# Performance work log

Measured on AMD Instinct MI355X. Metric: run time of the kernel, lower is better.

The kernel has to match this reference:

```python
import jax, jax.numpy as jnp
import numpy as np

IN_DIM = 256
HID = 384
HEADS = 6
NH1 = HID // HEADS  # 64 per-head hidden in layer1
N = 3072
SLOPE_GAT = 0.2   # LeakyReLU inside GAT attention
SLOPE_ACT = 0.01  # default nn.LeakyReLU / F.leaky_relu slope


def _leaky(x, s):
    return jnp.where(x >= 0, x, s * x)


def _gat_sublayer(h, mask, W, a, heads, nh, concat):
    # h: [N, F_in], mask: [N, N] bool, W: [heads*nh, F_in], a: [2*nh]
    n = h.shape[0]
    g = (h @ W.T).reshape(n, heads, nh)  # [N, H, F]
    # e[i,j,h] = leakyrelu(<g_i, a_l> + <g_j, a_r>)  (avoids O(N^2) concat)
    sl = jnp.einsum('nhf,f->nh', g, a[:nh])
    sr = jnp.einsum('nhf,f->nh', g, a[nh:])
    e = _leaky(sl[:, None, :] + sr[None, :, :], SLOPE_GAT)  # [N, N, H]
    e = jnp.where(mask[:, :, None], e, jnp.float32(-10000.0))
    att = jax.nn.softmax(e, axis=1)  # softmax over source nodes j
    out = jnp.einsum('ijh,jhf->ihf', att, g)
    return out.reshape(n, heads * nh) if concat else out.mean(axis=1)


def _gat(x, mask, W1, a1, W2, a2):
    x = _gat_sublayer(x, mask, W1, a1, HEADS, NH1, True)   # [N, HID]
    x = jax.nn.elu(x)
    return _gat_sublayer(x, mask, W2, a2, 1, IN_DIM, False)  # [N, IN_DIM]


def setup_inputs() -> dict:
    key = jax.random.key(0)
    ks = iter(jax.random.split(key, 32))
    d = {
        'feature': jax.random.normal(next(ks), (1, N, IN_DIM), jnp.float32),
        'adj': jax.random.randint(next(ks), (1, N, N), 0, 2, jnp.int32),
        'doc_num': 16,
        'sect_num': 192,
    }
    def w(shape, scale=0.05):
        return jax.random.normal(next(ks), shape, jnp.float32) * scale
    for br in ('sent', 'sect', 'doc'):
        d[f'W1_{br}'] = w((HID, IN_DIM))
        d[f'a1_{br}'] = w((2 * NH1,))
        d[f'W2_{br}'] = w((IN_DIM, HID))
        d[f'a2_{br}'] = w((2 * IN_DIM,))
    d['fusion_W'] = w((IN_DIM, 3 * IN_DIM)); d['fusion_b'] = jnp.zeros((IN_DIM,), jnp.float32)
    d['ffn_W0'] = w((HID, IN_DIM)); d['ffn_b0'] = jnp.zeros((HID,), jnp.float32)
    d['ffn_W1'] = w((HID, HID)); d['ffn_b1'] = jnp.zeros((HID,), jnp.float32)
    d['ffn_W2'] = w((IN_DIM, HID)); d['ffn_b2'] = jnp.zeros((IN_DIM,), jnp.float32)
    return d


def reference(feature, adj, doc_num, sect_num,
              W1_sent, a1_sent, W2_sent, a2_sent,
              W1_sect, a1_sect, W2_sect, a2_sect,
              W1_doc, a1_doc, W2_doc, a2_doc,
              fusion_W, fusion_b,
              ffn_W0, ffn_b0, ffn_W1, ffn_b1, ffn_W2, ffn_b2):
    f = feature[0]          # [N, D]
    n = f.shape[0]
    A = adj[0] != 0         # [N, N]
    cols = jnp.arange(n)
    sent_mask = A & (cols < n - sect_num - doc_num)[None, :]
    sect_mask = A & (cols >= n - sect_num - doc_num)[None, :] & (cols < n - doc_num)[None, :]
    doc_mask = A & (cols >= n - doc_num)[None, :]

    f_sent = _gat(f, sent_mask, W1_sent, a1_sent, W2_sent, a2_sent) + f
    f_sect = _gat(f, sect_mask, W1_sect, a1_sect, W2_sect, a2_sect) + f
    f_doc = _gat(f, doc_mask, W1_doc, a1_doc, W2_doc, a2_doc) + f

    fused = jnp.concatenate([f_doc, f_sect, f_sent], axis=-1)  # [N, 3D]
    fused = _leaky(fused @ fusion_W.T + fusion_b, SLOPE_ACT)
    h = _leaky(fused @ ffn_W0.T + ffn_b0, SLOPE_ACT)
    h = _leaky(h @ ffn_W1.T + ffn_b1, SLOPE_ACT)
    h = _leaky(h @ ffn_W2.T + ffn_b2, SLOPE_ACT)
    return (h + f)[None]    # [1, N, D]
```

## Files before the change

### kernel.cpp

```cpp
#include <hip/hip_runtime.h>
#include <stdint.h>

#define N_NODES 3072
#define D_IN    256
#define HIDDEN  384
#define HEADS   6
#define NH1     64
#define C1      1152
#define C2      768
#define MASK_ULL   48
#define MASK_BYTES 384
#define MASK_BSTRIDE ((size_t)N_NODES * MASK_BYTES)
#define CHUNK   2048
#define MAXQ    2
#define LOG2E   1.4426950408889634f

typedef __bf16 bf16;
typedef __bf16 bf16x8 __attribute__((ext_vector_type(8)));
typedef __bf16 bf16x4 __attribute__((ext_vector_type(4)));
typedef float  f32x4  __attribute__((ext_vector_type(4)));

__device__ __forceinline__ void atomAddF(float* p, float v) {
  __hip_atomic_fetch_add(p, v, __ATOMIC_RELAXED, __HIP_MEMORY_SCOPE_AGENT);
}
__device__ __forceinline__ float fexp2(float x) {
  float r; asm("v_exp_f32 %0, %1" : "=v"(r) : "v"(x)); return r;
}

struct CastArgs {
  const float* src[11];
  bf16*        dst[11];
  int          cum4[12];
};

__global__ __launch_bounds__(256) void cast_all_kernel(CastArgs A) {
  int g = blockIdx.x * 256 + threadIdx.x;
  int j = 0;
#pragma unroll
  for (int k = 1; k < 11; ++k) j += (g >= A.cum4[k]);
  int e = (g - A.cum4[j]) * 4;
  float4 v = *(const float4*)(A.src[j] + e);
  bf16x4 o = { (bf16)v.x, (bf16)v.y, (bf16)v.z, (bf16)v.w };
  *(bf16x4*)(A.dst[j] + e) = o;
}

__global__ __launch_bounds__(256) void pack_adj_kernel(const int* __restrict__ adj,
                                                       unsigned long long* __restrict__ maskU,
                                                       const int* __restrict__ dnum,
                                                       const int* __restrict__ snum) {
  int dn = dnum[0], sn = snum[0];
  int bb1 = N_NODES - sn - dn, bb2 = N_NODES - dn;
  int row = blockIdx.x;
  const int* ar = adj + (size_t)row * N_NODES;
  int lane = threadIdx.x & 63, wave = threadIdx.x >> 6;
#pragma unroll
  for (int it = 0; it < N_NODES / 256; ++it) {
    int j = it * 256 + wave * 64 + lane;
    bool a = ar[j] != 0;
    unsigned long long m0 = __ballot(a && (j < bb1));
    unsigned long long m1 = __ballot(a && (j >= bb1) && (j < bb2));
    unsigned long long m2 = __ballot(a && (j >= bb2));
    if (lane == 0) {
      size_t o = (size_t)row * MASK_ULL + it * 4 + wave;
      maskU[o] = m0;
      maskU[o + (size_t)N_NODES * MASK_ULL] = m1;
      maskU[o + 2 * (size_t)N_NODES * MASK_ULL] = m2;
    }
  }
}

template<int C>
__global__ __launch_bounds__(256) void pack_kernel(const bf16* __restrict__ src,
                                                   bf16* __restrict__ dst) {
  __shared__ bf16 t[64][72];
  int j0 = blockIdx.x * 64, f0 = blockIdx.y * 64;
  int rr = threadIdx.x >> 4;
  int cc = (threadIdx.x & 15) * 4;
#pragma unroll
  for (int p = 0; p < 4; ++p) {
    int r = p * 16 + rr;
    *(bf16x4*)&t[r][cc] = *(const bf16x4*)&src[(size_t)(j0 + r) * C + f0 + cc];
  }
  __syncthreads();
  int f = threadIdx.x & 63, g = threadIdx.x >> 6;
#pragma unroll
  for (int q = 0; q < 2; ++q) {
    int p = g * 2 + q;
    bf16x8 v = { t[p*8+0][f], t[p*8+1][f], t[p*8+2][f], t[p*8+3][f],
                 t[p*8+4][f], t[p*8+5][f], t[p*8+6][f], t[p*8+7][f] };
    *(bf16x8*)&dst[ ((size_t)((j0 >> 3) + p) * C + f0 + f) * 8 ] = v;
  }
}

template<int NHEADS, int NH>
__global__ __launch_bounds__(256) void head_proj_kernel(
    const bf16* __restrict__ g, int ldg,
    const float* __restrict__ a0, const float* __restrict__ a1, const float* __restrict__ a2,
    float* __restrict__ sl, float* __restrict__ sr) {
  int tid = blockIdx.x * 256 + threadIdx.x;
  int c = tid / N_NODES, i = tid - c * N_NODES;
  int b = c / NHEADS, h = c - b * NHEADS;
  const float* a = (b == 0) ? a0 : (b == 1) ? a1 : a2;
  const bf16* gr = g + (size_t)i * ldg + b * (NHEADS * NH) + h * NH;
  float accl = 0.f, accr = 0.f;
#pragma unroll 4
  for (int f = 0; f < NH; f += 4) {
    bf16x4 v = *(const bf16x4*)&gr[f];
#pragma unroll
    for (int k = 0; k < 4; ++k) {
      float gv = (float)v[k];
      accl += gv * a[f + k];
      accr += gv * a[NH + f + k];
    }
  }
  sl[c * N_NODES + i] = accl * LOG2E;
  sr[c * N_NODES + i] = accr * LOG2E;
}

__global__ __launch_bounds__(256) void colmean_kernel(const bf16* __restrict__ g, int C,
                                                      float* __restrict__ out) {
  int c = blockIdx.x * 256 + threadIdx.x;
  if (c >= C) return;
  int r0 = blockIdx.y * 128;
  float s = 0.f;
  for (int r = r0; r < r0 + 128; ++r) s += (float)g[(size_t)r * C + c];
  atomAddF(&out[c], s * (1.0f / N_NODES));
}

template<bool BIAS, bool LEAKY, bool RES, bool F32OUT>
__global__ __launch_bounds__(256) void gemm64_kernel(
    const bf16* __restrict__ A, int lda, int aZoff,
    const bf16* __restrict__ B0, const bf16* __restrict__ B1, const bf16* __restrict__ B2,
    int ldb, void* __restrict__ Cout, int ldc, int cZoff, int K,
    const float* __restrict__ bias, const float* __restrict__ res) {
  __shared__ bf16 As[64 * 64];
  __shared__ bf16 Bs[64 * 64];
  int z = blockIdx.z;
  const bf16* Ab = A + (size_t)z * aZoff;
  const bf16* Bb = (z == 0) ? B0 : (z == 1) ? B1 : B2;
  int m0 = blockIdx.x * 64, n0 = blockIdx.y * 64;
  int tid = threadIdx.x;
  int lane = tid & 63, wave = tid >> 6;
  int wm = wave >> 1, wn = wave & 1;
  int l15 = lane & 15, lk = lane >> 4;
  f32x4 acc[2][2] = {};
  for (int kt = 0; kt < K; kt += 64) {
#pragma unroll
    for (int h = 0; h < 2; ++h) {
      int u = h * 256 + tid;
      int r = u >> 3, up = u & 7;
      int ul = up ^ (r & 7);
      *(bf16x8*)&As[r * 64 + up * 8] = *(const bf16x8*)&Ab[(size_t)(m0 + r) * lda + kt + ul * 8];
      *(bf16x8*)&Bs[r * 64 + up * 8] = *(const bf16x8*)&Bb[(size_t)(n0 + r) * ldb + kt + ul * 8];
    }
    __syncthreads();
#pragma unroll
    for (int s = 0; s < 2; ++s) {
      bf16x8 af[2], bfr[2];
      int u = s * 4 + lk;
#pragma unroll
      for (int mi = 0; mi < 2; ++mi) {
        int r = wm * 32 + mi * 16 + l15;
        af[mi] = *(const bf16x8*)&As[r * 64 + (u ^ (r & 7)) * 8];
      }
#pragma unroll
      for (int ni = 0; ni < 2; ++ni) {
        int r = wn * 32 + ni * 16 + l15;
        bfr[ni] = *(const bf16x8*)&Bs[r * 64 + (u ^ (r & 7)) * 8];
      }
#pragma unroll
      for (int mi = 0; mi < 2; ++mi)
#pragma unroll
        for (int ni = 0; ni < 2; ++ni)
          acc[mi][ni] = __builtin_amdgcn_mfma_f32_16x16x32_bf16(af[mi], bfr[ni], acc[mi][ni], 0, 0, 0);
    }
    __syncthreads();
  }
#pragma unroll
  for (int mi = 0; mi < 2; ++mi)
#pragma unroll
    for (int ni = 0; ni < 2; ++ni)
#pragma unroll
      for (int r = 0; r < 4; ++r) {
        int i = m0 + wm * 32 + mi * 16 + lk * 4 + r;
        int col = z * cZoff + n0 + wn * 32 + ni * 16 + l15;
        float v = acc[mi][ni][r];
        if (BIAS) v += bias[col];
        if (LEAKY) v = (v >= 0.f) ? v : 0.01f * v;
        if (RES) v += res[(size_t)i * ldc + col];
        if (F32OUT) ((float*)Cout)[(size_t)i * ldc + col] = v;
        else        ((bf16*)Cout)[(size_t)i * ldc + col] = (bf16)v;
      }
}

template<bool L1>
__global__ __launch_bounds__(256) void att_kernel(
    const bf16* __restrict__ gP, const float* __restrict__ slA, const float* __restrict__ srA,
    const unsigned char* __restrict__ maskB,
    const int* __restrict__ dnum, const int* __restrict__ snum,
    float* __restrict__ accP, float* __restrict__ lP) {
  constexpr int C = L1 ? C1 : C2;
  int c = blockIdx.y;
  int b = L1 ? (c / 6) : (c >> 2);
  int colbase = L1 ? c * 64 : (b * 256 + (c & 3) * 64);
  int sidx = L1 ? c : b;
  int q = blockIdx.z;
  int dn = dnum[0], sn = snum[0];
  int bb1 = N_NODES - sn - dn, bb2 = N_NODES - dn;
  int jlo = (b == 0) ? 0 : (b == 1) ? bb1 : bb2;
  int jhi = (b == 0) ? bb1 : (b == 1) ? bb2 : N_NODES;
  int lo32 = jlo & ~31, hi32 = (jhi + 31) & ~31;
  int qlo = q * CHUNK, qhi = qlo + CHUNK;
  if (lo32 >= qhi || hi32 <= qlo) return;

  int wave = threadIdx.x >> 6, lane = threadIdx.x & 63;
  int l15 = lane & 15, lk = lane >> 4;
  int i0 = blockIdx.x * 16;
  int wlo = max(lo32, qlo + wave * (CHUNK / 4));
  int whi = min(hi32, qlo + (wave + 1) * (CHUNK / 4));
  int ip = i0 + l15;
  float sl = slA[sidx * N_NODES + ip];
  const float* srp = srA + sidx * N_NODES;
  const unsigned char* mrow = maskB + (size_t)b * MASK_BSTRIDE + (size_t)ip * MASK_BYTES;
  f32x4 acc[4] = {};
  float lsum = 0.f;
  for (int jt = wlo; jt < whi; jt += 32) {
    int jb = jt + lk * 8;
    unsigned int mb = mrow[jb >> 3];
    float4 s0 = *(const float4*)&srp[jb];
    float4 s1 = *(const float4*)&srp[jb + 4];
    float sv[8] = { s0.x, s0.y, s0.z, s0.w, s1.x, s1.y, s1.z, s1.w };
    bf16x8 a8;
#pragma unroll
    for (int e = 0; e < 8; ++e) {
      float x = sl + sv[e];
      x = fmaxf(x, 0.f) + 0.2f * fminf(x, 0.f);
      float p = fexp2(x);
      p = ((mb >> e) & 1u) ? p : 0.f;
      a8[e] = (bf16)p;
      lsum += p;
    }
    size_t pbase = (size_t)(jb >> 3) * C * 8;
#pragma unroll
    for (int nf = 0; nf < 4; ++nf) {
      bf16x8 b8 = *(const bf16x8*)&gP[pbase + (size_t)(colbase + nf * 16 + l15) * 8];
      acc[nf] = __builtin_amdgcn_mfma_f32_16x16x32_bf16(a8, b8, acc[nf], 0, 0, 0);
    }
  }
  lsum += __shfl_xor(lsum, 16, 64);
  lsum += __shfl_xor(lsum, 32, 64);

  __shared__ float red[4][16][64];
  __shared__ float redl[4][16];
#pragma unroll
  for (int nf = 0; nf < 4; ++nf)
#pragma unroll
    for (int r = 0; r < 4; ++r)
      red[wave][lk * 4 + r][nf * 16 + l15] = acc[nf][r];
  if (lane < 16) redl[wave][lane] = lsum;
  __syncthreads();
  int t = threadIdx.x;
  const float* rp = &red[0][0][0];
  f32x4 v = *(const f32x4*)(rp + t * 4);
  v += *(const f32x4*)(rp + 1024 + t * 4);
  v += *(const f32x4*)(rp + 2048 + t * 4);
  v += *(const f32x4*)(rp + 3072 + t * 4);
  int row = t >> 4, colg = (t & 15) * 4;
  int slot = c * MAXQ + q;
  *(f32x4*)&accP[((size_t)slot * N_NODES + i0 + row) * 64 + colg] = v;
  if (t < 16)
    lP[(size_t)slot * N_NODES + i0 + t] = redl[0][t] + redl[1][t] + redl[2][t] + redl[3][t];
}

__global__ __launch_bounds__(256) void fin1_kernel(
    const float* __restrict__ accP, const float* __restrict__ lP,
    const float* __restrict__ gm, const int* __restrict__ dnum, const int* __restrict__ snum,
    bf16* __restrict__ out1) {
  int t = blockIdx.x * 256 + threadIdx.x;
  int i = t / (C1 / 8), f0 = (t - i * (C1 / 8)) * 8;
  int c = f0 >> 6;
  int b = c / 6;
  int dn = dnum[0], sn = snum[0];
  int bb1 = N_NODES - sn - dn, bb2 = N_NODES - dn;
  int jlo = (b == 0) ? 0 : (b == 1) ? bb1 : bb2;
  int jhi = (b == 0) ? bb1 : (b == 1) ? bb2 : N_NODES;
  float l = 0.f;
  float a[8] = {0.f,0.f,0.f,0.f,0.f,0.f,0.f,0.f};
  if (jhi > jlo) {
    int q0 = jlo >> 11, q1 = (jhi - 1) >> 11;
    for (int q = q0; q <= q1; ++q) {
      int slot = c * MAXQ + q;
      l += lP[(size_t)slot * N_NODES + i];
      const float* ap = &accP[((size_t)slot * N_NODES + i) * 64 + (f0 & 63)];
      f32x4 v0 = *(const f32x4*)ap, v1 = *(const f32x4*)(ap + 4);
#pragma unroll
      for (int e = 0; e < 4; ++e) { a[e] += v0[e]; a[e + 4] += v1[e]; }
    }
  }
  float inv = (l > 0.f) ? 1.f / l : 0.f;
  bf16x8 o;
#pragma unroll
  for (int e = 0; e < 8; ++e) {
    float v = (l > 0.f) ? a[e] * inv : gm[f0 + e];
    v = (v > 0.f) ? v : (__expf(v) - 1.f);
    o[e] = (bf16)v;
  }
  *(bf16x8*)&out1[(size_t)i * C1 + f0] = o;
}

__global__ __launch_bounds__(256) void fin2_kernel(
    const float* __restrict__ accP, const float* __restrict__ lP,
    const float* __restrict__ gm, const float* __restrict__ feat,
    const int* __restrict__ dnum, const int* __restrict__ snum,
    bf16* __restrict__ fused) {
  int t = blockIdx.x * 256 + threadIdx.x;
  int i = t / (C2 / 8), f0 = (t - i * (C2 / 8)) * 8;
  int b = f0 >> 8;
  int fi = f0 & 255;
  int fc = (f0 >> 6) & 3;
  int c = b * 4 + fc;
  int dn = dnum[0], sn = snum[0];
  int bb1 = N_NODES - sn - dn, bb2 = N_NODES - dn;
  int jlo = (b == 0) ? 0 : (b == 1) ? bb1 : bb2;
  int jhi = (b == 0) ? bb1 : (b == 1) ? bb2 : N_NODES;
  float l = 0.f;
  float a[8] = {0.f,0.f,0.f,0.f,0.f,0.f,0.f,0.f};
  if (jhi > jlo) {
    int q0 = jlo >> 11, q1 = (jhi - 1) >> 11;
    for (int q = q0; q <= q1; ++q) {
      int slot = c * MAXQ + q;
      l += lP[(size_t)slot * N_NODES + i];
      const float* ap = &accP[((size_t)slot * N_NODES + i) * 64 + (f0 & 63)];
      f32x4 v0 = *(const f32x4*)ap, v1 = *(const f32x4*)(ap + 4);
#pragma unroll
      for (int e = 0; e < 4; ++e) { a[e] += v0[e]; a[e + 4] += v1[e]; }
    }
  }
  float inv = (l > 0.f) ? 1.f / l : 0.f;
  bf16x8 o;
#pragma unroll
  for (int e = 0; e < 8; ++e) {
    float v = (l > 0.f) ? a[e] * inv : gm[f0 + e];
    v += feat[(size_t)i * D_IN + fi + e];
    o[e] = (bf16)v;
  }
  *(bf16x8*)&fused[(size_t)i * C2 + (2 - b) * D_IN + fi] = o;
}

extern "C" void kernel_launch(void* const* d_in, const int* in_sizes, int n_in,
                              void* d_out, int out_size, void* d_ws, size_t ws_size,
                              hipStream_t stream) {
  (void)in_sizes; (void)n_in; (void)out_size; (void)ws_size;
  const float* feature = (const float*)d_in[0];
  const int*   adj     = (const int*)d_in[1];
  const int*   dnum    = (const int*)d_in[2];
  const int*   snum    = (const int*)d_in[3];
  const float* W1s = (const float*)d_in[4];  const float* a1s = (const float*)d_in[5];
  const float* W2s = (const float*)d_in[6];  const float* a2s = (const float*)d_in[7];
  const float* W1e = (const float*)d_in[8];  const float* a1e = (const float*)d_in[9];
  const float* W2e = (const float*)d_in[10]; const float* a2e = (const float*)d_in[11];
  const float* W1d = (const float*)d_in[12]; const float* a1d = (const float*)d_in[13];
  const float* W2d = (const float*)d_in[14]; const float* a2d = (const float*)d_in[15];
  const float* fW  = (const float*)d_in[16]; const float* fB  = (const float*)d_in[17];
  const float* w0  = (const float*)d_in[18]; const float* b0  = (const float*)d_in[19];
  const float* w1  = (const float*)d_in[20]; const float* b1  = (const float*)d_in[21];
  const float* w2  = (const float*)d_in[22]; const float* b2  = (const float*)d_in[23];

  char* ws = (char*)d_ws;
  size_t off = 0;
  auto alloc = [&](size_t bytes) { void* p = ws + off; off += (bytes + 255) & ~(size_t)255; return p; };

  unsigned long long* maskU = (unsigned long long*)alloc(3 * (size_t)N_NODES * MASK_ULL * 8);
  bf16* fbf   = (bf16*)alloc((size_t)N_NODES * D_IN * 2);
  bf16* w1b0  = (bf16*)alloc(HIDDEN * D_IN * 2);
  bf16* w1b1  = (bf16*)alloc(HIDDEN * D_IN * 2);
  bf16* w1b2  = (bf16*)alloc(HIDDEN * D_IN * 2);
  bf16* w2b0  = (bf16*)alloc(D_IN * HIDDEN * 2);
  bf16* w2b1  = (bf16*)alloc(D_IN * HIDDEN * 2);
  bf16* w2b2  = (bf16*)alloc(D_IN * HIDDEN * 2);
  bf16* wfusb = (bf16*)alloc(D_IN * C2 * 2);
  bf16* wf0b  = (bf16*)alloc(HIDDEN * D_IN * 2);
  bf16* wf1b  = (bf16*)alloc(HIDDEN * HIDDEN * 2);
  bf16* wf2b  = (bf16*)alloc(D_IN * HIDDEN * 2);
  bf16* g1    = (bf16*)alloc((size_t)N_NODES * C1 * 2);
  bf16* gP1   = (bf16*)alloc((size_t)N_NODES * C1 * 2);
  bf16* out1  = (bf16*)alloc((size_t)N_NODES * C1 * 2);
  bf16* g2    = (bf16*)alloc((size_t)N_NODES * C2 * 2);
  bf16* gP2   = (bf16*)alloc((size_t)N_NODES * C2 * 2);
  bf16* fusedB= (bf16*)alloc((size_t)N_NODES * C2 * 2);
  bf16* h0    = (bf16*)alloc((size_t)N_NODES * D_IN * 2);
  bf16* h1    = (bf16*)alloc((size_t)N_NODES * HIDDEN * 2);
  bf16* h2    = (bf16*)alloc((size_t)N_NODES * HIDDEN * 2);
  float* sl1  = (float*)alloc(18 * N_NODES * 4);
  float* sr1  = (float*)alloc(18 * N_NODES * 4);
  float* sl2  = (float*)alloc(3 * N_NODES * 4);
  float* sr2  = (float*)alloc(3 * N_NODES * 4);
  float* accU = (float*)alloc((size_t)18 * MAXQ * N_NODES * 64 * 4);
  float* lU   = (float*)alloc((size_t)18 * MAXQ * N_NODES * 4);
  size_t zoff = off;
  float* gm1  = (float*)alloc(C1 * 4);
  float* gm2  = (float*)alloc(C2 * 4);
  size_t zbytes = off - zoff;
  const unsigned char* maskBytes = (const unsigned char*)maskU;

  hipMemsetAsync(ws + zoff, 0, zbytes, stream);

  CastArgs ca;
  {
    const float* srcs[11] = { feature, W1s, W1e, W1d, W2s, W2e, W2d, fW, w0, w1, w2 };
    bf16* dsts[11] = { fbf, w1b0, w1b1, w1b2, w2b0, w2b1, w2b2, wfusb, wf0b, wf1b, wf2b };
    int counts[11] = { N_NODES*D_IN, HIDDEN*D_IN, HIDDEN*D_IN, HIDDEN*D_IN,
                       D_IN*HIDDEN, D_IN*HIDDEN, D_IN*HIDDEN, D_IN*C2,
                       HIDDEN*D_IN, HIDDEN*HIDDEN, D_IN*HIDDEN };
    int cum = 0;
    for (int k = 0; k < 11; ++k) { ca.src[k] = srcs[k]; ca.dst[k] = dsts[k]; ca.cum4[k] = cum; cum += counts[k] / 4; }
    ca.cum4[11] = cum;
    cast_all_kernel<<<cum / 256, 256, 0, stream>>>(ca);
  }
  pack_adj_kernel<<<N_NODES, 256, 0, stream>>>(adj, maskU, dnum, snum);
  gemm64_kernel<false,false,false,false><<<dim3(48,6,3), 256, 0, stream>>>(
      fbf, D_IN, 0, w1b0, w1b1, w1b2, D_IN, g1, C1, HIDDEN, D_IN, nullptr, nullptr);
  pack_kernel<C1><<<dim3(48,18), 256, 0, stream>>>(g1, gP1);
  head_proj_kernel<HEADS, NH1><<<18 * N_NODES / 256, 256, 0, stream>>>(g1, C1, a1s, a1e, a1d, sl1, sr1);
  colmean_kernel<<<dim3((C1 + 255) / 256, 24), 256, 0, stream>>>(g1, C1, gm1);
  att_kernel<true><<<dim3(192, 18, MAXQ), 256, 0, stream>>>(gP1, sl1, sr1, maskBytes, dnum, snum, accU, lU);
  fin1_kernel<<<N_NODES * (C1 / 8) / 256, 256, 0, stream>>>(accU, lU, gm1, dnum, snum, out1);
  gemm64_kernel<false,false,false,false><<<dim3(48,4,3), 256, 0, stream>>>(
      out1, C1, HIDDEN, w2b0, w2b1, w2b2, HIDDEN, g2, C2, D_IN, HIDDEN, nullptr, nullptr);
  pack_kernel<C2><<<dim3(48,12), 256, 0, stream>>>(g2, gP2);
  head_proj_kernel<1, D_IN><<<3 * N_NODES / 256, 256, 0, stream>>>(g2, C2, a2s, a2e, a2d, sl2, sr2);
  colmean_kernel<<<dim3((C2 + 255) / 256, 24), 256, 0, stream>>>(g2, C2, gm2);
  att_kernel<false><<<dim3(192, 12, MAXQ), 256, 0, stream>>>(gP2, sl2, sr2, maskBytes, dnum, snum, accU, lU);
  fin2_kernel<<<N_NODES * (C2 / 8) / 256, 256, 0, stream>>>(accU, lU, gm2, feature, dnum, snum, fusedB);
  gemm64_kernel<true,true,false,false><<<dim3(48,4,1), 256, 0, stream>>>(
      fusedB, C2, 0, wfusb, wfusb, wfusb, C2, h0, D_IN, 0, C2, fB, nullptr);
  gemm64_kernel<true,true,false,false><<<dim3(48,6,1), 256, 0, stream>>>(
      h0, D_IN, 0, wf0b, wf0b, wf0b, D_IN, h1, HIDDEN, 0, D_IN, b0, nullptr);
  gemm64_kernel<true,true,false,false><<<dim3(48,6,1), 256, 0, stream>>>(
      h1, HIDDEN, 0, wf1b, wf1b, wf1b, HIDDEN, h2, HIDDEN, 0, HIDDEN, b1, nullptr);
  gemm64_kernel<true,true,true,true><<<dim3(48,4,1), 256, 0, stream>>>(
      h2, HIDDEN, 0, wf2b, wf2b, wf2b, HIDDEN, d_out, D_IN, 0, HIDDEN, b2, feature);
}
```

Measured before the change: 327.7 us.

## Give each attention wave its own row tile and drop the LDS cross-wave reduction

The attention kernel previously split each 16-row tile's j-range across four waves and then merged their partial sums through shared memory with a barrier. Now each wave owns a separate 16-row tile and walks the full j-chunk itself, writing its results directly. The chunk size drops to 1536 so the two q-chunks split the range evenly, and the grid shrinks accordingly. The row-sum is now computed with an extra MFMA against a ones vector instead of scalar adds and shuffles, and LeakyReLU becomes a single fma. The trade-off is fewer blocks, longer per-wave loops and scattered stores, and the row-sum is now accumulated from the bf16-rounded weights rather than the fp32 values, a small precision change.

```diff
diff --git a/kernel.cpp b/kernel.cpp
--- a/kernel.cpp
+++ b/kernel.cpp
@@ -11,7 +11,7 @@
 #define MASK_ULL   48
 #define MASK_BYTES 384
 #define MASK_BSTRIDE ((size_t)N_NODES * MASK_BYTES)
-#define CHUNK   2048
+#define CHUNK   1536
 #define MAXQ    2
 #define LOG2E   1.4426950408889634f
 
@@ -211,19 +211,21 @@
   int jhi = (b == 0) ? bb1 : (b == 1) ? bb2 : N_NODES;
   int lo32 = jlo & ~31, hi32 = (jhi + 31) & ~31;
   int qlo = q * CHUNK, qhi = qlo + CHUNK;
-  if (lo32 >= qhi || hi32 <= qlo) return;
+  int wlo = max(lo32, qlo), whi = min(hi32, qhi);
+  if (wlo >= whi) return;
 
   int wave = threadIdx.x >> 6, lane = threadIdx.x & 63;
   int l15 = lane & 15, lk = lane >> 4;
-  int i0 = blockIdx.x * 16;
-  int wlo = max(lo32, qlo + wave * (CHUNK / 4));
-  int whi = min(hi32, qlo + (wave + 1) * (CHUNK / 4));
-  int ip = i0 + l15;
+  int row0 = blockIdx.x * 64 + wave * 16;
+  int ip = row0 + l15;
   float sl = slA[sidx * N_NODES + ip];
   const float* srp = srA + sidx * N_NODES;
   const unsigned char* mrow = maskB + (size_t)b * MASK_BSTRIDE + (size_t)ip * MASK_BYTES;
+  bf16x8 ones;
+#pragma unroll
+  for (int e = 0; e < 8; ++e) ones[e] = (bf16)1.0f;
   f32x4 acc[4] = {};
-  float lsum = 0.f;
+  f32x4 accl = {};
   for (int jt = wlo; jt < whi; jt += 32) {
     int jb = jt + lk * 8;
     unsigned int mb = mrow[jb >> 3];
@@ -234,11 +236,10 @@
 #pragma unroll
     for (int e = 0; e < 8; ++e) {
       float x = sl + sv[e];
-      x = fmaxf(x, 0.f) + 0.2f * fminf(x, 0.f);
+      x = fmaf(fminf(x, 0.f), -0.8f, x);
       float p = fexp2(x);
       p = ((mb >> e) & 1u) ? p : 0.f;
       a8[e] = (bf16)p;
-      lsum += p;
     }
     size_t pbase = (size_t)(jb >> 3) * C * 8;
 #pragma unroll
@@ -246,30 +247,20 @@
       bf16x8 b8 = *(const bf16x8*)&gP[pbase + (size_t)(colbase + nf * 16 + l15) * 8];
       acc[nf] = __builtin_amdgcn_mfma_f32_16x16x32_bf16(a8, b8, acc[nf], 0, 0, 0);
     }
-  }
-  lsum += __shfl_xor(lsum, 16, 64);
-  lsum += __shfl_xor(lsum, 32, 64);
-
-  __shared__ float red[4][16][64];
-  __shared__ float redl[4][16];
+    accl = __builtin_amdgcn_mfma_f32_16x16x32_bf16(a8, ones, accl, 0, 0, 0);
+  }
+  int slot = c * MAXQ + q;
+  float* ap = accP + ((size_t)slot * N_NODES + row0) * 64;
 #pragma unroll
   for (int nf = 0; nf < 4; ++nf)
 #pragma unroll
     for (int r = 0; r < 4; ++r)
-      red[wave][lk * 4 + r][nf * 16 + l15] = acc[nf][r];
-  if (lane < 16) redl[wave][lane] = lsum;
-  __syncthreads();
-  int t = threadIdx.x;
-  const float* rp = &red[0][0][0];
-  f32x4 v = *(const f32x4*)(rp + t * 4);
-  v += *(const f32x4*)(rp + 1024 + t * 4);
-  v += *(const f32x4*)(rp + 2048 + t * 4);
-  v += *(const f32x4*)(rp + 3072 + t * 4);
-  int row = t >> 4, colg = (t & 15) * 4;
-  int slot = c * MAXQ + q;
-  *(f32x4*)&accP[((size_t)slot * N_NODES + i0 + row) * 64 + colg] = v;
-  if (t < 16)
-    lP[(size_t)slot * N_NODES + i0 + t] = redl[0][t] + redl[1][t] + redl[2][t] + redl[3][t];
+      ap[(lk * 4 + r) * 64 + nf * 16 + l15] = acc[nf][r];
+  if (l15 == 0) {
+#pragma unroll
+    for (int r = 0; r < 4; ++r)
+      lP[(size_t)slot * N_NODES + row0 + lk * 4 + r] = accl[r];
+  }
 }
 
 __global__ __launch_bounds__(256) void fin1_kernel(
@@ -287,7 +278,7 @@
   float l = 0.f;
   float a[8] = {0.f,0.f,0.f,0.f,0.f,0.f,0.f,0.f};
   if (jhi > jlo) {
-    int q0 = jlo >> 11, q1 = (jhi - 1) >> 11;
+    int q0 = jlo / CHUNK, q1 = (jhi - 1) / CHUNK;
     for (int q = q0; q <= q1; ++q) {
       int slot = c * MAXQ + q;
       l += lP[(size_t)slot * N_NODES + i];
@@ -326,7 +317,7 @@
   float l = 0.f;
   float a[8] = {0.f,0.f,0.f,0.f,0.f,0.f,0.f,0.f};
   if (jhi > jlo) {
-    int q0 = jlo >> 11, q1 = (jhi - 1) >> 11;
+    int q0 = jlo / CHUNK, q1 = (jhi - 1) / CHUNK;
     for (int q = q0; q <= q1; ++q) {
       int slot = c * MAXQ + q;
       l += lP[(size_t)slot * N_NODES + i];
@@ -423,14 +414,14 @@
   pack_kernel<C1><<<dim3(48,18), 256, 0, stream>>>(g1, gP1);
   head_proj_kernel<HEADS, NH1><<<18 * N_NODES / 256, 256, 0, stream>>>(g1, C1, a1s, a1e, a1d, sl1, sr1);
   colmean_kernel<<<dim3((C1 + 255) / 256, 24), 256, 0, stream>>>(g1, C1, gm1);
-  att_kernel<true><<<dim3(192, 18, MAXQ), 256, 0, stream>>>(gP1, sl1, sr1, maskBytes, dnum, snum, accU, lU);
+  att_kernel<true><<<dim3(48, 18, MAXQ), 256, 0, stream>>>(gP1, sl1, sr1, maskBytes, dnum, snum, accU, lU);
   fin1_kernel<<<N_NODES * (C1 / 8) / 256, 256, 0, stream>>>(accU, lU, gm1, dnum, snum, out1);
   gemm64_kernel<false,false,false,false><<<dim3(48,4,3), 256, 0, stream>>>(
       out1, C1, HIDDEN, w2b0, w2b1, w2b2, HIDDEN, g2, C2, D_IN, HIDDEN, nullptr, nullptr);
   pack_kernel<C2><<<dim3(48,12), 256, 0, stream>>>(g2, gP2);
   head_proj_kernel<1, D_IN><<<3 * N_NODES / 256, 256, 0, stream>>>(g2, C2, a2s, a2e, a2d, sl2, sr2);
   colmean_kernel<<<dim3((C2 + 255) / 256, 24), 256, 0, stream>>>(g2, C2, gm2);
-  att_kernel<false><<<dim3(192, 12, MAXQ), 256, 0, stream>>>(gP2, sl2, sr2, maskBytes, dnum, snum, accU, lU);
+  att_kernel<false><<<dim3(48, 12, MAXQ), 256, 0, stream>>>(gP2, sl2, sr2, maskBytes, dnum, snum, accU, lU);
   fin2_kernel<<<N_NODES * (C2 / 8) / 256, 256, 0, stream>>>(accU, lU, gm2, feature, dnum, snum, fusedB);
   gemm64_kernel<true,true,false,false><<<dim3(48,4,1), 256, 0, stream>>>(
       fusedB, C2, 0, wfusb, wfusb, wfusb, C2, h0, D_IN, 0, C2, fB, nullptr);
```

Result: faster. 310.9 us (-5.2%).
